# Kernel optimization log

Measured on AMD Instinct MI355X. Metric: run time of the kernel, lower is better.

Reference implementation:

```python
import jax, jax.numpy as jnp
import numpy as np

N_NODES = 50000
N_EDGES = 800000
IN_CH = 128
HID = 128
OUT_CH = 16
N_LAYERS = 3
N_GRAPHS = 128
BN_EPS = 1e-5


def setup_inputs() -> dict:
    key = jax.random.key(0)
    ks = jax.random.split(key, 12)
    x = jax.random.normal(ks[0], (N_NODES, IN_CH), dtype=jnp.float32)
    edge_index = jax.random.randint(ks[1], (2, N_EDGES), 0, N_NODES, dtype=jnp.int64)
    batch = jnp.sort(jax.random.randint(ks[2], (N_NODES,), 0, N_GRAPHS, dtype=jnp.int64))
    s = 1.0 / np.sqrt(HID)
    W1 = jax.random.normal(ks[3], (N_LAYERS, IN_CH, HID), dtype=jnp.float32) * s
    b1 = jax.random.normal(ks[4], (N_LAYERS, HID), dtype=jnp.float32) * s
    W2 = jax.random.normal(ks[5], (N_LAYERS, HID, HID), dtype=jnp.float32) * s
    b2 = jax.random.normal(ks[6], (N_LAYERS, HID), dtype=jnp.float32) * s
    gamma = jnp.ones((N_LAYERS, HID), dtype=jnp.float32)
    beta = jnp.zeros((N_LAYERS, HID), dtype=jnp.float32)
    mean = jax.random.normal(ks[7], (N_LAYERS, HID), dtype=jnp.float32) * 0.1
    var = jax.random.uniform(ks[8], (N_LAYERS, HID), dtype=jnp.float32, minval=0.5, maxval=1.5)
    Wc = jax.random.normal(ks[9], (HID, OUT_CH), dtype=jnp.float32) * s
    bc = jax.random.normal(ks[10], (OUT_CH,), dtype=jnp.float32) * s
    return {"x": x, "edge_index": edge_index, "batch": batch, "W1": W1, "b1": b1,
            "W2": W2, "b2": b2, "gamma": gamma, "beta": beta, "mean": mean,
            "var": var, "Wc": Wc, "bc": bc}


def reference(x, edge_index, batch, W1, b1, W2, b2, gamma, beta, mean, var, Wc, bc):
    # GIN (eval mode: BN uses running stats, dropout is identity).
    src, dst = edge_index[0], edge_index[1]
    n = x.shape[0]
    h = x
    for i in range(N_LAYERS):
        # GINConv with eps=0: MLP(x + sum_{j->i} x_j)
        agg = jax.ops.segment_sum(h[src], dst, num_segments=n)  # [N, d]
        z = h + agg
        z = jnp.maximum(z @ W1[i] + b1[i], 0.0) @ W2[i] + b2[i]  # 2-layer MLP
        # BatchNorm1d (eval) + ReLU
        inv = gamma[i] * jax.lax.rsqrt(var[i] + BN_EPS)
        h = jnp.maximum((z - mean[i]) * inv + beta[i], 0.0)
    pooled = jax.ops.segment_sum(h, batch, num_segments=N_GRAPHS)  # [G, hid]
    return pooled @ Wc + bc
```

## Files before the change

### kernel.cpp

```cpp
#include <hip/hip_runtime.h>

#define N_NODES 50000
#define N_EDGES 800000
#define CH 128
#define N_GRAPHS 128
#define N_LAYERS 3
#define OUT_CH 16
#define BN_EPS 1e-5f
#define ZN N_NODES
#define NB 196
#define BCAP 4608
#define PBCAP 8448
#define EPB 4096
#define NTILES (N_NODES / 16)
#define SSTRIDE 20
#define CB 6250
#define PB 388

typedef unsigned short ushort_t;
typedef __attribute__((ext_vector_type(8))) short bf16x8;
typedef __attribute__((ext_vector_type(8))) unsigned short u16x8;
typedef __attribute__((ext_vector_type(4))) float f32x4;

__device__ inline ushort_t f2b(float f) {
    unsigned u = __float_as_uint(f);
    unsigned r = (u + 0x7fffu + ((u >> 16) & 1u)) >> 16;
    return (ushort_t)r;
}
__device__ inline float blo(unsigned u) { return __uint_as_float(u << 16); }
__device__ inline float bhi(unsigned u) { return __uint_as_float(u & 0xffff0000u); }

__global__ __launch_bounds__(256) void setup_kernel(
    const float4* __restrict__ x, ushort4* __restrict__ xb, ushort4* __restrict__ xz,
    int* __restrict__ gcur, float* __restrict__ pooled,
    const float* __restrict__ W1, const float* __restrict__ W2, ushort_t* __restrict__ Wt,
    const float* __restrict__ b1, const float* __restrict__ b2,
    const float* __restrict__ gamma, const float* __restrict__ beta,
    const float* __restrict__ mean, const float* __restrict__ var,
    float* __restrict__ scale, float* __restrict__ shift) {
    int bid = blockIdx.x, t = threadIdx.x;
    if (bid < CB) {
        int i = bid * 256 + t;
        if (i < NB) gcur[i] = 0;
        if (i < N_GRAPHS * CH) pooled[i] = 0.f;
        if (bid == 0 && t < 32) {
            ushort4 zz; zz.x = 0; zz.y = 0; zz.z = 0; zz.w = 0;
            xb[(size_t)ZN * 32 + t] = zz;
            xz[(size_t)ZN * 32 + t] = zz;
        }
        float4 v = x[i];
        ushort4 o;
        o.x = f2b(v.x); o.y = f2b(v.y); o.z = f2b(v.z); o.w = f2b(v.w);
        xb[i] = o;
    } else {
        int i = (bid - CB) * 256 + t;
        if (i < 6 * CH * CH) {
            int mat = i >> 14, r = i & 16383;
            int j = r & 7, bb = r >> 3;
            int lane = bb & 63, cs = bb >> 6;
            int ct = cs >> 2, ks = cs & 3;
            int n = ct * 16 + (lane & 15);
            int k = ks * 32 + (lane >> 4) * 8 + j;
            const float* Wsrc = (mat < 3) ? (W1 + (size_t)mat * CH * CH)
                                          : (W2 + (size_t)(mat - 3) * CH * CH);
            Wt[i] = f2b(Wsrc[k * CH + n]);
        } else {
            int e = i - 6 * CH * CH;
            if (e >= 6 * CH) return;
            int mat = e / CH, c = e % CH;
            if (mat < 3) {
                scale[e] = 1.f;
                shift[e] = b1[mat * CH + c];
            } else {
                int l = mat - 3;
                float inv = gamma[l * CH + c] * rsqrtf(var[l * CH + c] + BN_EPS);
                scale[e] = inv;
                shift[e] = (b2[l * CH + c] - mean[l * CH + c]) * inv + beta[l * CH + c];
            }
        }
    }
}

__global__ __launch_bounds__(256) void bin_kernel(const int* __restrict__ src,
                                                  const int* __restrict__ dst,
                                                  int* __restrict__ gcur,
                                                  unsigned* __restrict__ gbuck) {
    __shared__ int lcnt[256];
    __shared__ int lpref[256];
    __shared__ int lpos[NB];
    __shared__ int lbase[NB];
    __shared__ unsigned stage[EPB];
    __shared__ unsigned char sbk[EPB];
    int t = threadIdx.x;
    int e0 = blockIdx.x * EPB;
    int nloc = N_EDGES - e0; if (nloc > EPB) nloc = EPB;

    lcnt[t] = 0;
    __syncthreads();

    int2 ed[16];
    #pragma unroll
    for (int j = 0; j < 16; ++j) {
        int i = j * 256 + t;
        if (i < nloc) {
            ed[j].x = src[e0 + i];
            ed[j].y = dst[e0 + i];
            atomicAdd(&lcnt[ed[j].y >> 8], 1);
        } else ed[j].y = -1;
    }
    __syncthreads();
    int v = lcnt[t];
    lpref[t] = v;
    __syncthreads();
    for (int off = 1; off < 256; off <<= 1) {
        int y = (t >= off) ? lpref[t - off] : 0;
        __syncthreads();
        lpref[t] += y;
        __syncthreads();
    }
    int excl = lpref[t] - v;
    __syncthreads();
    lpref[t] = excl;
    if (t < NB) {
        lpos[t] = excl;
        lbase[t] = atomicAdd(&gcur[t], v);
    }
    __syncthreads();
    #pragma unroll
    for (int j = 0; j < 16; ++j) {
        if (ed[j].y >= 0) {
            int b = ed[j].y >> 8;
            int slot = atomicAdd(&lpos[b], 1);
            stage[slot] = (unsigned)ed[j].x | ((unsigned)(ed[j].y & 255) << 16);
            sbk[slot] = (unsigned char)b;
        }
    }
    __syncthreads();
    for (int i = t; i < nloc; i += 256) {
        int b = sbk[i];
        gbuck[(size_t)b * BCAP + lbase[b] + (i - lpref[b])] = stage[i];
    }
}

__global__ __launch_bounds__(256) void place_kernel(const int* __restrict__ gcur,
                                                    const unsigned* __restrict__ gbuck,
                                                    int* __restrict__ rowptr,
                                                    ushort_t* __restrict__ esrc) {
    __shared__ ushort_t ssrc[BCAP];
    __shared__ unsigned char sd[BCAP];
    __shared__ ushort_t outS[PBCAP];
    __shared__ int cnt[256], pref[256], cur[256];
    int b = blockIdx.x, t = threadIdx.x;
    cnt[t] = 0;
    __syncthreads();
    int nb = gcur[b];
    for (int i = t; i < nb; i += 256) {
        unsigned p = gbuck[(size_t)b * BCAP + i];
        ssrc[i] = (ushort_t)(p & 0xffffu);
        int dl = (p >> 16) & 0xff;
        sd[i] = (unsigned char)dl;
        atomicAdd(&cnt[dl], 1);
    }
    __syncthreads();
    int v = cnt[t];
    int pc = (v + 15) & ~15;
    pref[t] = pc;
    __syncthreads();
    for (int off = 1; off < 256; off <<= 1) {
        int y = (t >= off) ? pref[t - off] : 0;
        __syncthreads();
        pref[t] += y;
        __syncthreads();
    }
    int excl = pref[t] - pc;
    int total = pref[255];
    __syncthreads();
    pref[t] = excl;
    cur[t] = 0;
    int idx = (b << 8) + t;
    if (idx < N_NODES)
        rowptr[idx] = (b * PBCAP + excl) | ((pc >> 4) << 24);
    __syncthreads();
    for (int i = t; i < total; i += 256) outS[i] = (ushort_t)ZN;
    __syncthreads();
    for (int i = t; i < nb; i += 256) {
        int dl = sd[i];
        int p = pref[dl] + atomicAdd(&cur[dl], 1);
        outS[p] = ssrc[i];
    }
    __syncthreads();
    for (int i = t; i < total; i += 256)
        esrc[(size_t)b * PBCAP + i] = outS[i];
}

__global__ __launch_bounds__(512, 8) void layer_kernel(
    const unsigned* __restrict__ h2, const int* __restrict__ rowptr,
    const ushort_t* __restrict__ esrc,
    const ushort_t* __restrict__ Wf1, const ushort_t* __restrict__ Wf2,
    const float* __restrict__ shift1, const float* __restrict__ scale2,
    const float* __restrict__ shift2, ushort_t* __restrict__ hout,
    const int* __restrict__ batch, float* __restrict__ pooled, int do_pool) {
    __shared__ unsigned zt[16][68];
    __shared__ ushort_t sS[CH * SSTRIDE];

    int t = threadIdx.x;
    int wave = t >> 6, lane = t & 63;
    int quad = lane >> 4, l16 = lane & 15;
    int row0 = blockIdx.x * 16;

    for (int nn = 0; nn < 2; ++nn) {
        int node = row0 + wave * 2 + nn;
        unsigned self = h2[(size_t)node * 64 + lane];
        float ax = blo(self), ay = bhi(self);
        int pr = rowptr[node];
        int e = pr & 0xFFFFFF;
        int rounds = (int)((unsigned)pr >> 24);
        for (int r = 0; r < rounds; ++r, e += 16) {
            u16x8 i0 = *(const u16x8*)(esrc + e);
            u16x8 i1 = *(const u16x8*)(esrc + e + 8);
            unsigned u[16];
            #pragma unroll
            for (int j = 0; j < 8; ++j)
                u[j] = h2[(size_t)i0[j] * 64 + lane];
            #pragma unroll
            for (int j = 0; j < 8; ++j)
                u[8 + j] = h2[(size_t)i1[j] * 64 + lane];
            #pragma unroll
            for (int j = 0; j < 16; ++j) { ax += blo(u[j]); ay += bhi(u[j]); }
        }
        zt[wave * 2 + nn][lane] = ((unsigned)f2b(ay) << 16) | (unsigned)f2b(ax);
    }
    __syncthreads();

    {
        bf16x8 af[4];
        #pragma unroll
        for (int ks = 0; ks < 4; ++ks)
            af[ks] = *(const bf16x8*)((const ushort_t*)&zt[l16][0] + ks * 32 + quad * 8);
        bf16x8 w1[4];
        #pragma unroll
        for (int ks = 0; ks < 4; ++ks)
            w1[ks] = *(const bf16x8*)(Wf1 + ((size_t)(wave * 4 + ks) * 64 + lane) * 8);
        f32x4 acc = (f32x4){0.f, 0.f, 0.f, 0.f};
        #pragma unroll
        for (int ks = 0; ks < 4; ++ks)
            acc = __builtin_amdgcn_mfma_f32_16x16x32_bf16(af[ks], w1[ks], acc, 0, 0, 0);
        int k = wave * 16 + l16;
        float sh = shift1[k];
        uint2 p;
        p.x = ((unsigned)f2b(fmaxf(acc[1] + sh, 0.f)) << 16)
            |  (unsigned)f2b(fmaxf(acc[0] + sh, 0.f));
        p.y = ((unsigned)f2b(fmaxf(acc[3] + sh, 0.f)) << 16)
            |  (unsigned)f2b(fmaxf(acc[2] + sh, 0.f));
        *(uint2*)&sS[k * SSTRIDE + quad * 4] = p;
    }
    __syncthreads();

    {
        bf16x8 af2[4];
        #pragma unroll
        for (int ks = 0; ks < 4; ++ks)
            #pragma unroll
            for (int j = 0; j < 8; ++j)
                af2[ks][j] = (short)sS[(ks * 32 + quad * 8 + j) * SSTRIDE + l16];
        bf16x8 w2[4];
        #pragma unroll
        for (int ks = 0; ks < 4; ++ks)
            w2[ks] = *(const bf16x8*)(Wf2 + ((size_t)(wave * 4 + ks) * 64 + lane) * 8);
        f32x4 acc = (f32x4){0.f, 0.f, 0.f, 0.f};
        #pragma unroll
        for (int ks = 0; ks < 4; ++ks)
            acc = __builtin_amdgcn_mfma_f32_16x16x32_bf16(af2[ks], w2[ks], acc, 0, 0, 0);
        int col = wave * 16 + l16;
        float sc = scale2[col], sh = shift2[col];
        float hv[4];
        #pragma unroll
        for (int r = 0; r < 4; ++r)
            hv[r] = fmaxf(acc[r] * sc + sh, 0.f);
        if (!do_pool) {
            #pragma unroll
            for (int r = 0; r < 4; ++r) {
                int row = row0 + quad * 4 + r;
                hout[(size_t)row * CH + col] = f2b(hv[r]);
            }
        } else {
            int g0 = batch[row0], g15 = batch[row0 + 15];
            if (g0 == g15) {
                float s = hv[0] + hv[1] + hv[2] + hv[3];
                s += __shfl_xor(s, 16);
                s += __shfl_xor(s, 32);
                if (quad == 0) atomicAdd(&pooled[g0 * CH + col], s);
            } else {
                #pragma unroll
                for (int r = 0; r < 4; ++r) {
                    int row = row0 + quad * 4 + r;
                    atomicAdd(&pooled[batch[row] * CH + col], hv[r]);
                }
            }
        }
    }
}

__global__ __launch_bounds__(256) void cls_kernel(const float* __restrict__ pooled,
                                                  const float* __restrict__ Wc,
                                                  const float* __restrict__ bc,
                                                  float* __restrict__ out) {
    int i = blockIdx.x * blockDim.x + threadIdx.x;
    if (i >= N_GRAPHS * OUT_CH) return;
    int g = i / OUT_CH, o = i % OUT_CH;
    float s = bc[o];
    for (int k = 0; k < CH; ++k) s += pooled[g * CH + k] * Wc[k * OUT_CH + o];
    out[i] = s;
}

extern "C" void kernel_launch(void* const* d_in, const int* in_sizes, int n_in,
                              void* d_out, int out_size, void* d_ws, size_t ws_size,
                              hipStream_t stream) {
    const float* x     = (const float*)d_in[0];
    const int*   eidx  = (const int*)d_in[1];
    const int*   batch = (const int*)d_in[2];
    const float* W1    = (const float*)d_in[3];
    const float* b1    = (const float*)d_in[4];
    const float* W2    = (const float*)d_in[5];
    const float* b2    = (const float*)d_in[6];
    const float* gamma = (const float*)d_in[7];
    const float* beta  = (const float*)d_in[8];
    const float* mean  = (const float*)d_in[9];
    const float* var   = (const float*)d_in[10];
    const float* Wc    = (const float*)d_in[11];
    const float* bc    = (const float*)d_in[12];
    float* out = (float*)d_out;

    const int* src = eidx;
    const int* dst = eidx + N_EDGES;

    char* w = (char*)d_ws;
    size_t off = 0;
    auto alloc = [&](size_t bytes) { void* p = w + off; off += (bytes + 255) & ~(size_t)255; return p; };
    int*      gcur   = (int*)alloc(NB * 4);
    unsigned* gbuck  = (unsigned*)alloc((size_t)NB * BCAP * 4);
    int*      rowptr = (int*)alloc(N_NODES * 4);
    ushort_t* esrc   = (ushort_t*)alloc((size_t)NB * PBCAP * 2);
    ushort_t* Bh     = (ushort_t*)alloc((size_t)(N_NODES + 1) * CH * 2);
    ushort_t* Bz     = (ushort_t*)alloc((size_t)(N_NODES + 1) * CH * 2);
    ushort_t* Wt     = (ushort_t*)alloc((size_t)6 * CH * CH * 2);
    float*    scale  = (float*)alloc(6 * CH * 4);
    float*    shift  = (float*)alloc(6 * CH * 4);
    float*    pooled = (float*)alloc(N_GRAPHS * CH * 4);
    (void)ws_size; (void)n_in; (void)in_sizes; (void)out_size;

    setup_kernel<<<CB + PB, 256, 0, stream>>>(
        (const float4*)x, (ushort4*)Bh, (ushort4*)Bz, gcur, pooled,
        W1, W2, Wt, b1, b2, gamma, beta, mean, var, scale, shift);
    bin_kernel<<<(N_EDGES + EPB - 1) / EPB, 256, 0, stream>>>(src, dst, gcur, gbuck);
    place_kernel<<<NB, 256, 0, stream>>>(gcur, gbuck, rowptr, esrc);

    ushort_t* bufA = Bh;
    ushort_t* bufB = Bz;
    for (int i = 0; i < N_LAYERS; ++i) {
        int last = (i == N_LAYERS - 1);
        layer_kernel<<<NTILES, 512, 0, stream>>>((const unsigned*)bufA, rowptr, esrc,
                                                 Wt + (size_t)i * CH * CH,
                                                 Wt + (size_t)(3 + i) * CH * CH,
                                                 shift + i * CH,
                                                 scale + (3 + i) * CH,
                                                 shift + (3 + i) * CH,
                                                 bufB, batch, pooled, last);
        ushort_t* tmp = bufA; bufA = bufB; bufB = tmp;
    }

    cls_kernel<<<(N_GRAPHS * OUT_CH + 255) / 256, 256, 0, stream>>>(pooled, Wc, bc, out);
}
```

Baseline: 230.4 us.

## Fuse edge binning into setup kernel and software-pipeline neighbor gathers

```diff
diff --git a/kernel.cpp b/kernel.cpp
--- a/kernel.cpp
+++ b/kernel.cpp
@@ -14,6 +14,7 @@
 #define EPB 4096
 #define NTILES (N_NODES / 16)
 #define SSTRIDE 20
+#define BINB 196
 #define CB 6250
 #define PB 388
 
@@ -30,20 +31,93 @@
 __device__ inline float blo(unsigned u) { return __uint_as_float(u << 16); }
 __device__ inline float bhi(unsigned u) { return __uint_as_float(u & 0xffff0000u); }
 
-__global__ __launch_bounds__(256) void setup_kernel(
+__global__ __launch_bounds__(256) void setup_bin_kernel(
+    const int* __restrict__ src, const int* __restrict__ dst,
+    int* __restrict__ gcur, unsigned* __restrict__ gbuck,
     const float4* __restrict__ x, ushort4* __restrict__ xb, ushort4* __restrict__ xz,
-    int* __restrict__ gcur, float* __restrict__ pooled,
+    float* __restrict__ pooled,
     const float* __restrict__ W1, const float* __restrict__ W2, ushort_t* __restrict__ Wt,
     const float* __restrict__ b1, const float* __restrict__ b2,
     const float* __restrict__ gamma, const float* __restrict__ beta,
     const float* __restrict__ mean, const float* __restrict__ var,
     float* __restrict__ scale, float* __restrict__ shift) {
     int bid = blockIdx.x, t = threadIdx.x;
-    if (bid < CB) {
-        int i = bid * 256 + t;
-        if (i < NB) gcur[i] = 0;
+    if (bid < BINB) {
+        __shared__ int lcnt[256];
+        __shared__ int lpref[256];
+        __shared__ int lpos[NB];
+        __shared__ int lbase[NB];
+        __shared__ unsigned stage[EPB];
+        __shared__ unsigned char sbk[EPB];
+        int e0 = bid * EPB;
+        int nloc = N_EDGES - e0; if (nloc > EPB) nloc = EPB;
+
+        lcnt[t] = 0;
+        __syncthreads();
+
+        int2 ed[16];
+        const int4* s4 = (const int4*)(src + e0);
+        const int4* d4 = (const int4*)(dst + e0);
+        #pragma unroll
+        for (int k = 0; k < 4; ++k) {
+            int base = k * 1024 + t * 4;
+            if (base + 3 < nloc) {
+                int4 sv = s4[k * 256 + t];
+                int4 dv = d4[k * 256 + t];
+                ed[k * 4 + 0].x = sv.x; ed[k * 4 + 0].y = dv.x;
+                ed[k * 4 + 1].x = sv.y; ed[k * 4 + 1].y = dv.y;
+                ed[k * 4 + 2].x = sv.z; ed[k * 4 + 2].y = dv.z;
+                ed[k * 4 + 3].x = sv.w; ed[k * 4 + 3].y = dv.w;
+            } else {
+                #pragma unroll
+                for (int m = 0; m < 4; ++m) {
+                    int i = base + m;
+                    if (i < nloc) {
+                        ed[k * 4 + m].x = src[e0 + i];
+                        ed[k * 4 + m].y = dst[e0 + i];
+                    } else ed[k * 4 + m].y = -1;
+                }
+            }
+        }
+        #pragma unroll
+        for (int j = 0; j < 16; ++j)
+            if (ed[j].y >= 0) atomicAdd(&lcnt[ed[j].y >> 8], 1);
+        __syncthreads();
+        int v = lcnt[t];
+        lpref[t] = v;
+        __syncthreads();
+        for (int off = 1; off < 256; off <<= 1) {
+            int y = (t >= off) ? lpref[t - off] : 0;
+            __syncthreads();
+            lpref[t] += y;
+            __syncthreads();
+        }
+        int excl = lpref[t] - v;
+        __syncthreads();
+        lpref[t] = excl;
+        if (t < NB) {
+            lpos[t] = excl;
+            lbase[t] = atomicAdd(&gcur[t], v);
+        }
+        __syncthreads();
+        #pragma unroll
+        for (int j = 0; j < 16; ++j) {
+            if (ed[j].y >= 0) {
+                int b = ed[j].y >> 8;
+                int slot = atomicAdd(&lpos[b], 1);
+                stage[slot] = (unsigned)ed[j].x | ((unsigned)(ed[j].y & 255) << 16);
+                sbk[slot] = (unsigned char)b;
+            }
+        }
+        __syncthreads();
+        for (int i = t; i < nloc; i += 256) {
+            int b = sbk[i];
+            gbuck[(size_t)b * BCAP + lbase[b] + (i - lpref[b])] = stage[i];
+        }
+    } else if (bid < BINB + CB) {
+        int i = (bid - BINB) * 256 + t;
         if (i < N_GRAPHS * CH) pooled[i] = 0.f;
-        if (bid == 0 && t < 32) {
+        if (bid == BINB && t < 32) {
             ushort4 zz; zz.x = 0; zz.y = 0; zz.z = 0; zz.w = 0;
             xb[(size_t)ZN * 32 + t] = zz;
             xz[(size_t)ZN * 32 + t] = zz;
@@ -53,7 +127,7 @@
         o.x = f2b(v.x); o.y = f2b(v.y); o.z = f2b(v.z); o.w = f2b(v.w);
         xb[i] = o;
     } else {
-        int i = (bid - CB) * 256 + t;
+        int i = (bid - BINB - CB) * 256 + t;
         if (i < 6 * CH * CH) {
             int mat = i >> 14, r = i & 16383;
             int j = r & 7, bb = r >> 3;
@@ -81,67 +155,6 @@
     }
 }
 
-__global__ __launch_bounds__(256) void bin_kernel(const int* __restrict__ src,
-                                                  const int* __restrict__ dst,
-                                                  int* __restrict__ gcur,
-                                                  unsigned* __restrict__ gbuck) {
-    __shared__ int lcnt[256];
-    __shared__ int lpref[256];
-    __shared__ int lpos[NB];
-    __shared__ int lbase[NB];
-    __shared__ unsigned stage[EPB];
-    __shared__ unsigned char sbk[EPB];
-    int t = threadIdx.x;
-    int e0 = blockIdx.x * EPB;
-    int nloc = N_EDGES - e0; if (nloc > EPB) nloc = EPB;
-
-    lcnt[t] = 0;
-    __syncthreads();
-
-    int2 ed[16];
-    #pragma unroll
-    for (int j = 0; j < 16; ++j) {
-        int i = j * 256 + t;
-        if (i < nloc) {
-            ed[j].x = src[e0 + i];
-            ed[j].y = dst[e0 + i];
-            atomicAdd(&lcnt[ed[j].y >> 8], 1);
-        } else ed[j].y = -1;
-    }
-    __syncthreads();
-    int v = lcnt[t];
-    lpref[t] = v;
-    __syncthreads();
-    for (int off = 1; off < 256; off <<= 1) {
-        int y = (t >= off) ? lpref[t - off] : 0;
-        __syncthreads();
-        lpref[t] += y;
-        __syncthreads();
-    }
-    int excl = lpref[t] - v;
-    __syncthreads();
-    lpref[t] = excl;
-    if (t < NB) {
-        lpos[t] = excl;
-        lbase[t] = atomicAdd(&gcur[t], v);
-    }
-    __syncthreads();
-    #pragma unroll
-    for (int j = 0; j < 16; ++j) {
-        if (ed[j].y >= 0) {
-            int b = ed[j].y >> 8;
-            int slot = atomicAdd(&lpos[b], 1);
-            stage[slot] = (unsigned)ed[j].x | ((unsigned)(ed[j].y & 255) << 16);
-            sbk[slot] = (unsigned char)b;
-        }
-    }
-    __syncthreads();
-    for (int i = t; i < nloc; i += 256) {
-        int b = sbk[i];
-        gbuck[(size_t)b * BCAP + lbase[b] + (i - lpref[b])] = stage[i];
-    }
-}
-
 __global__ __launch_bounds__(256) void place_kernel(const int* __restrict__ gcur,
                                                     const unsigned* __restrict__ gbuck,
                                                     int* __restrict__ rowptr,
@@ -208,27 +221,55 @@
     int quad = lane >> 4, l16 = lane & 15;
     int row0 = blockIdx.x * 16;
 
-    for (int nn = 0; nn < 2; ++nn) {
-        int node = row0 + wave * 2 + nn;
-        unsigned self = h2[(size_t)node * 64 + lane];
-        float ax = blo(self), ay = bhi(self);
-        int pr = rowptr[node];
-        int e = pr & 0xFFFFFF;
-        int rounds = (int)((unsigned)pr >> 24);
-        for (int r = 0; r < rounds; ++r, e += 16) {
+    {
+        int node0 = row0 + wave * 2;
+        unsigned self0 = h2[(size_t)node0 * 64 + lane];
+        unsigned self1 = h2[(size_t)(node0 + 1) * 64 + lane];
+        int pr0 = __builtin_amdgcn_readfirstlane(rowptr[node0]);
+        int pr1 = __builtin_amdgcn_readfirstlane(rowptr[node0 + 1]);
+        int e  = pr0 & 0xFFFFFF;
+        int rA = (int)((unsigned)pr0 >> 24);
+        int rounds = rA + (int)((unsigned)pr1 >> 24);
+        float ax = blo(self0), ay = bhi(self0);
+        float sx = 0.f, sy = 0.f;
+        unsigned ucur[16];
+        if (rounds > 0) {
             u16x8 i0 = *(const u16x8*)(esrc + e);
             u16x8 i1 = *(const u16x8*)(esrc + e + 8);
-            unsigned u[16];
             #pragma unroll
-            for (int j = 0; j < 8; ++j)
-                u[j] = h2[(size_t)i0[j] * 64 + lane];
+            for (int j = 0; j < 8; ++j) ucur[j] = h2[(size_t)i0[j] * 64 + lane];
             #pragma unroll
-            for (int j = 0; j < 8; ++j)
-                u[8 + j] = h2[(size_t)i1[j] * 64 + lane];
+            for (int j = 0; j < 8; ++j) ucur[8 + j] = h2[(size_t)i1[j] * 64 + lane];
+        }
+        for (int r = 0; r < rounds; ++r) {
+            unsigned un[16];
+            if (r + 1 < rounds) {
+                const ushort_t* ep = esrc + e + 16;
+                u16x8 i0 = *(const u16x8*)ep;
+                u16x8 i1 = *(const u16x8*)(ep + 8);
+                #pragma unroll
+                for (int j = 0; j < 8; ++j) un[j] = h2[(size_t)i0[j] * 64 + lane];
+                #pragma unroll
+                for (int j = 0; j < 8; ++j) un[8 + j] = h2[(size_t)i1[j] * 64 + lane];
+            }
+            if (r == rA) { sx = ax; sy = ay; ax = blo(self1); ay = bhi(self1); }
             #pragma unroll
-            for (int j = 0; j < 16; ++j) { ax += blo(u[j]); ay += bhi(u[j]); }
-        }
-        zt[wave * 2 + nn][lane] = ((unsigned)f2b(ay) << 16) | (unsigned)f2b(ax);
+            for (int j = 0; j < 16; ++j) { ax += blo(ucur[j]); ay += bhi(ucur[j]); }
+            if (r + 1 < rounds) {
+                #pragma unroll
+                for (int j = 0; j < 16; ++j) ucur[j] = un[j];
+            }
+            e += 16;
+        }
+        float bx, by;
+        if (rA == rounds) {
+            sx = ax; sy = ay;
+            bx = blo(self1); by = bhi(self1);
+        } else {
+            bx = ax; by = ay;
+        }
+        zt[wave * 2][lane]     = ((unsigned)f2b(sy) << 16) | (unsigned)f2b(sx);
+        zt[wave * 2 + 1][lane] = ((unsigned)f2b(by) << 16) | (unsigned)f2b(bx);
     }
     __syncthreads();
 
@@ -349,10 +390,11 @@
     float*    pooled = (float*)alloc(N_GRAPHS * CH * 4);
     (void)ws_size; (void)n_in; (void)in_sizes; (void)out_size;
 
-    setup_kernel<<<CB + PB, 256, 0, stream>>>(
-        (const float4*)x, (ushort4*)Bh, (ushort4*)Bz, gcur, pooled,
+    hipMemsetAsync(gcur, 0, NB * 4, stream);
+    setup_bin_kernel<<<BINB + CB + PB, 256, 0, stream>>>(
+        src, dst, gcur, gbuck,
+        (const float4*)x, (ushort4*)Bh, (ushort4*)Bz, pooled,
         W1, W2, Wt, b1, b2, gamma, beta, mean, var, scale, shift);
-    bin_kernel<<<(N_EDGES + EPB - 1) / EPB, 256, 0, stream>>>(src, dst, gcur, gbuck);
     place_kernel<<<NB, 256, 0, stream>>>(gcur, gbuck, rowptr, esrc);
 
     ushort_t* bufA = Bh;
```

Measured after the change: 261.7 us. +13.6%, slower.
